# Performance work log

Measured on AMD Instinct MI355X. Metric: run time of the kernel, lower is better.

## Reference

```python
import jax, jax.numpy as jnp
import numpy as np

B, NQ, NK, D = 4, 4096, 4096, 1024


def setup_inputs() -> dict:
    key = jax.random.key(0)
    kq, kv = jax.random.split(key)
    query = jax.random.normal(kq, (B, NQ, D), dtype=jnp.float32)
    values = jax.random.normal(kv, (B, NK, D), dtype=jnp.float32)
    return {"query": query, "values": values}


def reference(query, values):
    # scores = Q @ V^T  (unscaled), shape [B, NQ, NK]
    scores = jnp.einsum("bqd,bkd->bqk", query, values)
    attn = jax.nn.softmax(scores, axis=-1)
    # context = attn @ V, shape [B, NQ, D]
    context = jnp.einsum("bqk,bkd->bqd", attn, values)
    return context
```

## Files before the change

### kernel.cpp

```cpp
#include <hip/hip_runtime.h>


#define NB   4
#define NQL  4096
#define NKL  4096
#define DIM  1024
#define BQ   32
#define BK   32
#define NW   8
#define DSL  128
#define NT   (NKL / BK)
#define LOG2E 1.44269504088896340736f
#define PBW  40

typedef float f32x2 __attribute__((ext_vector_type(2)));
typedef float f32x4 __attribute__((ext_vector_type(4)));
typedef _Float16 f16x8 __attribute__((ext_vector_type(8)));
typedef short s16x8 __attribute__((ext_vector_type(8)));
typedef short s16x4 __attribute__((ext_vector_type(4)));
typedef unsigned int uint_;

union Frag { f16x8 v; s16x8 s; _Float16 h[8]; };

__device__ __forceinline__ void rawbar() {
    asm volatile("s_waitcnt lgkmcnt(0)\n\ts_barrier" ::: "memory");
}

__global__ void prep_v(const float* __restrict__ Vg, short* __restrict__ v16,
                       short* __restrict__ vt16) {
    __shared__ short lds[64][72];
    const int t   = (int)threadIdx.x;
    const int blk = (int)blockIdx.x;
    const int bb    = blk >> 10;
    const int ktile = (blk >> 4) & 63;
    const int dtile = blk & 15;
    const int k0 = ktile * 64, d0 = dtile * 64;
    const int row = t >> 2;
    const int cb  = (t & 3) * 16;

    const float* src = Vg + ((size_t)(bb * NKL + k0 + row) * DIM + d0 + cb);
    short* vdst = v16 + ((size_t)(bb * NKL + k0 + row) * DIM + d0 + cb);
#pragma unroll
    for (int i = 0; i < 4; ++i) {
        f32x4 x = *(const f32x4*)(src + i * 4);
        s16x4 h;
#pragma unroll
        for (int j = 0; j < 4; ++j)
            h[j] = __builtin_bit_cast(short, (_Float16)x[j]);
        *(s16x4*)(vdst + i * 4) = h;
        *(s16x4*)&lds[row][cb + i * 4] = h;
    }
    __syncthreads();
    short* tdst = vt16 + ((size_t)(bb * DIM + d0 + row) * NKL + k0 + cb);
#pragma unroll
    for (int i = 0; i < 4; ++i) {
        s16x4 h;
#pragma unroll
        for (int j = 0; j < 4; ++j)
            h[j] = lds[cb + i * 4 + j][row];
        *(s16x4*)(tdst + i * 4) = h;
    }
}

template<int MODE>
__global__ __attribute__((amdgpu_flat_work_group_size(512, 512),
                          amdgpu_waves_per_eu(1, 4)))
void attn_f16(const float* __restrict__ Qg, const float* __restrict__ Vg,
              float* __restrict__ Og, const short* __restrict__ v16,
              const short* __restrict__ vt16) {
    __shared__ float spart[2][NW][BQ][BK];
    __shared__ __align__(16) short pbuf[2][BQ * PBW];
    __shared__ float arun[2][BQ];
    __shared__ float lsum[BQ];

    const int tid = (int)threadIdx.x;
    const int l   = tid & 63;
    const int w   = tid >> 6;
    const int l15 = l & 15;
    const int lg  = l >> 4;

    const int bid  = (int)blockIdx.x;
    const int orig = (bid & 7) * 64 + (bid >> 3);
    const int b  = orig >> 7;
    const int qt = orig & 127;
    const int q0 = qt * BQ;
    const int dw = w * DSL;

    f16x8 qf[2][4];
#pragma unroll
    for (int qb = 0; qb < 2; ++qb)
#pragma unroll
        for (int dc = 0; dc < 4; ++dc) {
            const float* qp = Qg + (size_t)(b * NQL + q0 + qb * 16 + l15) * DIM
                            + dw + dc * 32 + lg * 8;
            f32x4 x0 = *(const f32x4*)qp;
            f32x4 x1 = *(const f32x4*)(qp + 4);
            f16x8 a;
#pragma unroll
            for (int j = 0; j < 4; ++j) { a[j] = (_Float16)x0[j]; a[j + 4] = (_Float16)x1[j]; }
            qf[qb][dc] = a;
        }

    f32x4 oacc[2][8];
#pragma unroll
    for (int qb = 0; qb < 2; ++qb)
#pragma unroll
        for (int dg = 0; dg < 8; ++dg)
            oacc[qb][dg] = (f32x4){0.f, 0.f, 0.f, 0.f};

    f32x4 sacc[2][2];
    f32x4 hA32[4][2], hB32[4][2];
    s16x8 hA16[4], hB16[4];

    auto loadstage = [&](int buf, int kt_, int kb) {
        if constexpr (MODE == 1) {
            const short* vp = v16 + ((size_t)(b * NKL + kt_ * BK + kb * 16 + l15) * DIM
                            + dw + lg * 8);
            s16x8 (&hb)[4] = buf ? hB16 : hA16;
#pragma unroll
            for (int dc = 0; dc < 4; ++dc)
                hb[dc] = *(const s16x8*)(vp + dc * 32);
        } else {
            const float* vp = Vg + (size_t)(b * NKL + kt_ * BK + kb * 16 + l15) * DIM
                            + dw + lg * 8;
            f32x4 (&hb)[4][2] = buf ? hB32 : hA32;
#pragma unroll
            for (int dc = 0; dc < 4; ++dc) {
                hb[dc][0] = *(const f32x4*)(vp + dc * 32);
                hb[dc][1] = *(const f32x4*)(vp + dc * 32 + 4);
            }
        }
    };

    auto qkt_half = [&](int buf, int kb) {
#pragma unroll
        for (int dc = 0; dc < 4; ++dc) {
            Frag fa;
            if constexpr (MODE == 1) {
                fa.s = buf ? hB16[dc] : hA16[dc];
            } else {
                f32x4 (&hb)[4][2] = buf ? hB32 : hA32;
#pragma unroll
                for (int j = 0; j < 4; ++j) {
                    fa.h[j]     = (_Float16)hb[dc][0][j];
                    fa.h[j + 4] = (_Float16)hb[dc][1][j];
                }
            }
            sacc[kb][0] = __builtin_amdgcn_mfma_f32_16x16x32_f16(fa.v, qf[0][dc], sacc[kb][0], 0, 0, 0);
            sacc[kb][1] = __builtin_amdgcn_mfma_f32_16x16x32_f16(fa.v, qf[1][dc], sacc[kb][1], 0, 0, 0);
        }
    };

    auto qkt_tile = [&](int kt_, int spbuf) {
#pragma unroll
        for (int kb = 0; kb < 2; ++kb)
#pragma unroll
            for (int qb = 0; qb < 2; ++qb)
                sacc[kb][qb] = (f32x4){0.f, 0.f, 0.f, 0.f};
        const int ktn = (kt_ + 1 < NT) ? kt_ + 1 : NT - 1;
        qkt_half(0, 0);
        loadstage(0, ktn, 0);
        qkt_half(1, 1);
        loadstage(1, ktn, 1);
#pragma unroll
        for (int kb = 0; kb < 2; ++kb)
#pragma unroll
            for (int qb = 0; qb < 2; ++qb) {
                const int q = qb * 16 + l15;
                const int kblk = (kb * 16 + lg * 4) ^ ((q & 7) << 2);
                *(f32x4*)&spart[spbuf][w][q][kblk] = sacc[kb][qb];
            }
    };

    const int qsm = 4 * w + lg;
    const int kk  = (2 * l15) ^ ((qsm & 7) << 2);

    float m_reg  = -3e38f;
    float l_lane = 0.f;

    auto softmax_tile = [&](int cur) {
        f32x2 sp = (f32x2){0.f, 0.f};
#pragma unroll
        for (int wv = 0; wv < NW; ++wv)
            sp += *(const f32x2*)&spart[cur][wv][qsm][kk];
        float s0 = sp[0], s1 = sp[1];
        float smax = fmaxf(s0, s1);
        float alpha = 1.0f;
        if (!__all(smax - m_reg <= 8.0f)) {
            float mloc = smax;
#pragma unroll
            for (int off = 1; off < 16; off <<= 1)
                mloc = fmaxf(mloc, __shfl_xor(mloc, off));
            float mnew = fmaxf(m_reg, mloc);
            alpha = exp2f((m_reg - mnew) * LOG2E);
            m_reg = mnew;
        }
        float p0 = exp2f((s0 - m_reg) * LOG2E);
        float p1 = exp2f((s1 - m_reg) * LOG2E);
        l_lane = alpha * l_lane + (p0 + p1);
        if (l15 == 0) arun[cur][qsm] = alpha;
        uint_ pk = (uint_)__builtin_bit_cast(unsigned short, (_Float16)p0)
                 | ((uint_)__builtin_bit_cast(unsigned short, (_Float16)p1) << 16);
        *(uint_*)&pbuf[cur][qsm * PBW + 2 * l15] = pk;
    };

    s16x8 pvreg[8];
    float pv32[8][8];

    auto pv_loads = [&](int kt_) {
        if constexpr (MODE == 1) {
            const short* vtb = vt16 + ((size_t)(b * DIM + dw + l15) * NKL
                             + kt_ * BK + lg * 8);
#pragma unroll
            for (int dg = 0; dg < 8; ++dg)
                pvreg[dg] = *(const s16x8*)(vtb + (size_t)dg * 16 * NKL);
        }
    };

    auto pv_tile = [&](int kt_, int cur) {
        if constexpr (MODE == 0) {
            const float* vb = Vg + (size_t)(b * NKL + kt_ * BK + lg * 8) * DIM
                            + dw + l15;
#pragma unroll
            for (int dg = 0; dg < 8; ++dg)
#pragma unroll
                for (int j = 0; j < 8; ++j)
                    pv32[dg][j] = vb[(size_t)j * DIM + dg * 16];
        }
        f32x4 av[2];
#pragma unroll
        for (int qb = 0; qb < 2; ++qb)
            av[qb] = *(const f32x4*)&arun[cur][qb * 16 + lg * 4];
        bool mine1 = true;
#pragma unroll
        for (int qb = 0; qb < 2; ++qb)
#pragma unroll
            for (int r = 0; r < 4; ++r)
                mine1 = mine1 && (av[qb][r] == 1.0f);
        if (!__all(mine1)) {
#pragma unroll
            for (int qb = 0; qb < 2; ++qb)
#pragma unroll
                for (int dg = 0; dg < 8; ++dg)
#pragma unroll
                    for (int r = 0; r < 4; ++r)
                        oacc[qb][dg][r] *= av[qb][r];
        }
        Frag pf[2];
#pragma unroll
        for (int qb = 0; qb < 2; ++qb)
            pf[qb].s = *(const s16x8*)&pbuf[cur][(qb * 16 + l15) * PBW + lg * 8];
#pragma unroll
        for (int dg = 0; dg < 8; ++dg) {
            Frag bf;
            if constexpr (MODE == 1) {
                bf.s = pvreg[dg];
            } else {
#pragma unroll
                for (int j = 0; j < 8; ++j)
                    bf.h[j] = (_Float16)pv32[dg][j];
            }
            __builtin_amdgcn_s_setprio(1);
#pragma unroll
            for (int qb = 0; qb < 2; ++qb)
                oacc[qb][dg] = __builtin_amdgcn_mfma_f32_16x16x32_f16(
                    pf[qb].v, bf.v, oacc[qb][dg], 0, 0, 0);
            __builtin_amdgcn_s_setprio(0);
        }
    };

    loadstage(0, 0, 0);
    loadstage(1, 0, 1);
    qkt_tile(0, 0);
    rawbar();

    for (int kt = 1; kt < NT; ++kt) {
        const int cur = (kt - 1) & 1;
        pv_loads(kt - 1);
        qkt_tile(kt, kt & 1);
        softmax_tile(cur);
        rawbar();
        pv_tile(kt - 1, cur);
    }

    {
        const int cur = (NT - 1) & 1;
        pv_loads(NT - 1);
        softmax_tile(cur);
        rawbar();
        pv_tile(NT - 1, cur);
    }

    {
        float rs = l_lane;
#pragma unroll
        for (int off = 1; off < 16; off <<= 1)
            rs += __shfl_xor(rs, off);
        if (l15 == 0) lsum[qsm] = rs;
    }
    __syncthreads();
#pragma unroll
    for (int qb = 0; qb < 2; ++qb) {
        f32x4 lv = *(const f32x4*)&lsum[qb * 16 + lg * 4];
        float il[4];
#pragma unroll
        for (int r = 0; r < 4; ++r) il[r] = 1.0f / lv[r];
#pragma unroll
        for (int dg = 0; dg < 8; ++dg)
#pragma unroll
            for (int r = 0; r < 4; ++r) {
                int q = q0 + qb * 16 + lg * 4 + r;
                int d = dw + dg * 16 + l15;
                Og[(size_t)(b * NQL + q) * DIM + d] = oacc[qb][dg][r] * il[r];
            }
    }
}

extern "C" void kernel_launch(void* const* d_in, const int* in_sizes, int n_in,
                              void* d_out, int out_size, void* d_ws, size_t ws_size,
                              hipStream_t stream) {
    const float* Q = (const float*)d_in[0];
    const float* V = (const float*)d_in[1];
    float* O = (float*)d_out;
    (void)in_sizes; (void)n_in; (void)out_size;

    const size_t elems = (size_t)NB * NKL * DIM;
    const size_t need  = 2 * elems * sizeof(short);
    dim3 grid(NB * (NQL / BQ));
    dim3 block(NW * 64);
    if (ws_size >= need) {
        short* v16  = (short*)d_ws;
        short* vt16 = v16 + elems;
        prep_v<<<dim3(NB * 1024), dim3(256), 0, stream>>>(V, v16, vt16);
        attn_f16<1><<<grid, block, 0, stream>>>(Q, V, O, v16, vt16);
    } else {
        attn_f16<0><<<grid, block, 0, stream>>>(Q, V, O, nullptr, nullptr);
    }
}
```

Baseline: 937.1 us.

## Double key tile to 64 and store partial scores in fp16 LDS

Raises the key tile from 32 to 64, so each iteration covers four 16-key QK^T sub-blocks and two PV k-chunks. This halves the number of loop iterations, barriers and softmax passes. Partial scores from each wave are now written to LDS as fp16 instead of fp32, halving LDS traffic for the cross-wave reduction, at the cost of precision in the partial sums. The second PV chunk is loaded inside pv_tile without prefetch, which may expose latency and adds register pressure.

```diff
diff --git a/kernel.cpp b/kernel.cpp
--- a/kernel.cpp
+++ b/kernel.cpp
@@ -6,21 +6,20 @@
 #define NKL  4096
 #define DIM  1024
 #define BQ   32
-#define BK   32
+#define BK   64
 #define NW   8
 #define DSL  128
 #define NT   (NKL / BK)
 #define LOG2E 1.44269504088896340736f
-#define PBW  40
-
-typedef float f32x2 __attribute__((ext_vector_type(2)));
+#define PBW  72
+
 typedef float f32x4 __attribute__((ext_vector_type(4)));
 typedef _Float16 f16x8 __attribute__((ext_vector_type(8)));
 typedef short s16x8 __attribute__((ext_vector_type(8)));
 typedef short s16x4 __attribute__((ext_vector_type(4)));
-typedef unsigned int uint_;
-
-union Frag { f16x8 v; s16x8 s; _Float16 h[8]; };
+
+union Frag  { f16x8 v; s16x8 s; _Float16 h[8]; };
+union Half4 { s16x4 s; _Float16 h[4]; };
 
 __device__ __forceinline__ void rawbar() {
     asm volatile("s_waitcnt lgkmcnt(0)\n\ts_barrier" ::: "memory");
@@ -68,7 +67,7 @@
 void attn_f16(const float* __restrict__ Qg, const float* __restrict__ Vg,
               float* __restrict__ Og, const short* __restrict__ v16,
               const short* __restrict__ vt16) {
-    __shared__ float spart[2][NW][BQ][BK];
+    __shared__ __align__(16) short spart_h[2][NW][BQ][BK];
     __shared__ __align__(16) short pbuf[2][BQ * PBW];
     __shared__ float arun[2][BQ];
     __shared__ float lsum[BQ];
@@ -108,26 +107,24 @@
         for (int dg = 0; dg < 8; ++dg)
             oacc[qb][dg] = (f32x4){0.f, 0.f, 0.f, 0.f};
 
-    f32x4 sacc[2][2];
-    f32x4 hA32[4][2], hB32[4][2];
-    s16x8 hA16[4], hB16[4];
+    f32x4 sacc[4][2];
+    s16x8 hst[2][4];
+    f32x4 hst32[2][4][2];
 
     auto loadstage = [&](int buf, int kt_, int kb) {
         if constexpr (MODE == 1) {
             const short* vp = v16 + ((size_t)(b * NKL + kt_ * BK + kb * 16 + l15) * DIM
                             + dw + lg * 8);
-            s16x8 (&hb)[4] = buf ? hB16 : hA16;
 #pragma unroll
             for (int dc = 0; dc < 4; ++dc)
-                hb[dc] = *(const s16x8*)(vp + dc * 32);
+                hst[buf][dc] = *(const s16x8*)(vp + dc * 32);
         } else {
             const float* vp = Vg + (size_t)(b * NKL + kt_ * BK + kb * 16 + l15) * DIM
                             + dw + lg * 8;
-            f32x4 (&hb)[4][2] = buf ? hB32 : hA32;
 #pragma unroll
             for (int dc = 0; dc < 4; ++dc) {
-                hb[dc][0] = *(const f32x4*)(vp + dc * 32);
-                hb[dc][1] = *(const f32x4*)(vp + dc * 32 + 4);
+                hst32[buf][dc][0] = *(const f32x4*)(vp + dc * 32);
+                hst32[buf][dc][1] = *(const f32x4*)(vp + dc * 32 + 4);
             }
         }
     };
@@ -137,13 +134,12 @@
         for (int dc = 0; dc < 4; ++dc) {
             Frag fa;
             if constexpr (MODE == 1) {
-                fa.s = buf ? hB16[dc] : hA16[dc];
+                fa.s = hst[buf][dc];
             } else {
-                f32x4 (&hb)[4][2] = buf ? hB32 : hA32;
 #pragma unroll
                 for (int j = 0; j < 4; ++j) {
-                    fa.h[j]     = (_Float16)hb[dc][0][j];
-                    fa.h[j + 4] = (_Float16)hb[dc][1][j];
+                    fa.h[j]     = (_Float16)hst32[buf][dc][0][j];
+                    fa.h[j + 4] = (_Float16)hst32[buf][dc][1][j];
                 }
             }
             sacc[kb][0] = __builtin_amdgcn_mfma_f32_16x16x32_f16(fa.v, qf[0][dc], sacc[kb][0], 0, 0, 0);
@@ -153,38 +149,46 @@
 
     auto qkt_tile = [&](int kt_, int spbuf) {
 #pragma unroll
-        for (int kb = 0; kb < 2; ++kb)
+        for (int kb = 0; kb < 4; ++kb)
 #pragma unroll
             for (int qb = 0; qb < 2; ++qb)
                 sacc[kb][qb] = (f32x4){0.f, 0.f, 0.f, 0.f};
         const int ktn = (kt_ + 1 < NT) ? kt_ + 1 : NT - 1;
-        qkt_half(0, 0);
-        loadstage(0, ktn, 0);
-        qkt_half(1, 1);
-        loadstage(1, ktn, 1);
-#pragma unroll
-        for (int kb = 0; kb < 2; ++kb)
+        qkt_half(0, 0);  loadstage(0, kt_, 2);
+        qkt_half(1, 1);  loadstage(1, kt_, 3);
+        qkt_half(0, 2);  loadstage(0, ktn, 0);
+        qkt_half(1, 3);  loadstage(1, ktn, 1);
+#pragma unroll
+        for (int kb = 0; kb < 4; ++kb)
 #pragma unroll
             for (int qb = 0; qb < 2; ++qb) {
                 const int q = qb * 16 + l15;
                 const int kblk = (kb * 16 + lg * 4) ^ ((q & 7) << 2);
-                *(f32x4*)&spart[spbuf][w][q][kblk] = sacc[kb][qb];
+                Half4 pk;
+#pragma unroll
+                for (int r = 0; r < 4; ++r)
+                    pk.h[r] = (_Float16)sacc[kb][qb][r];
+                *(s16x4*)&spart_h[spbuf][w][q][kblk] = pk.s;
             }
     };
 
     const int qsm = 4 * w + lg;
-    const int kk  = (2 * l15) ^ ((qsm & 7) << 2);
+    const int kk  = (4 * l15) ^ ((qsm & 7) << 2);
 
     float m_reg  = -3e38f;
     float l_lane = 0.f;
 
     auto softmax_tile = [&](int cur) {
-        f32x2 sp = (f32x2){0.f, 0.f};
-#pragma unroll
-        for (int wv = 0; wv < NW; ++wv)
-            sp += *(const f32x2*)&spart[cur][wv][qsm][kk];
-        float s0 = sp[0], s1 = sp[1];
-        float smax = fmaxf(s0, s1);
+        float s[4] = {0.f, 0.f, 0.f, 0.f};
+#pragma unroll
+        for (int wv = 0; wv < NW; ++wv) {
+            Half4 hp;
+            hp.s = *(const s16x4*)&spart_h[cur][wv][qsm][kk];
+#pragma unroll
+            for (int r = 0; r < 4; ++r)
+                s[r] += (float)hp.h[r];
+        }
+        float smax = fmaxf(fmaxf(s[0], s[1]), fmaxf(s[2], s[3]));
         float alpha = 1.0f;
         if (!__all(smax - m_reg <= 8.0f)) {
             float mloc = smax;
@@ -195,17 +199,20 @@
             alpha = exp2f((m_reg - mnew) * LOG2E);
             m_reg = mnew;
         }
-        float p0 = exp2f((s0 - m_reg) * LOG2E);
-        float p1 = exp2f((s1 - m_reg) * LOG2E);
-        l_lane = alpha * l_lane + (p0 + p1);
+        float psum = 0.f;
+        Half4 pk;
+#pragma unroll
+        for (int r = 0; r < 4; ++r) {
+            float p = exp2f((s[r] - m_reg) * LOG2E);
+            psum += p;
+            pk.h[r] = (_Float16)p;
+        }
+        l_lane = alpha * l_lane + psum;
         if (l15 == 0) arun[cur][qsm] = alpha;
-        uint_ pk = (uint_)__builtin_bit_cast(unsigned short, (_Float16)p0)
-                 | ((uint_)__builtin_bit_cast(unsigned short, (_Float16)p1) << 16);
-        *(uint_*)&pbuf[cur][qsm * PBW + 2 * l15] = pk;
+        *(s16x4*)&pbuf[cur][qsm * PBW + 4 * l15] = pk.s;
     };
 
     s16x8 pvreg[8];
-    float pv32[8][8];
 
     auto pv_loads = [&](int kt_) {
         if constexpr (MODE == 1) {
@@ -218,14 +225,13 @@
     };
 
     auto pv_tile = [&](int kt_, int cur) {
-        if constexpr (MODE == 0) {
-            const float* vb = Vg + (size_t)(b * NKL + kt_ * BK + lg * 8) * DIM
-                            + dw + l15;
+        s16x8 pv1[8];
+        if constexpr (MODE == 1) {
+            const short* vtb = vt16 + ((size_t)(b * DIM + dw + l15) * NKL
+                             + kt_ * BK + lg * 8);
 #pragma unroll
             for (int dg = 0; dg < 8; ++dg)
-#pragma unroll
-                for (int j = 0; j < 8; ++j)
-                    pv32[dg][j] = vb[(size_t)j * DIM + dg * 16];
+                pv1[dg] = *(const s16x8*)(vtb + (size_t)dg * 16 * NKL + 32);
         }
         f32x4 av[2];
 #pragma unroll
@@ -246,26 +252,49 @@
                     for (int r = 0; r < 4; ++r)
                         oacc[qb][dg][r] *= av[qb][r];
         }
-        Frag pf[2];
+        Frag pf[2][2];
 #pragma unroll
         for (int qb = 0; qb < 2; ++qb)
-            pf[qb].s = *(const s16x8*)&pbuf[cur][(qb * 16 + l15) * PBW + lg * 8];
-#pragma unroll
-        for (int dg = 0; dg < 8; ++dg) {
-            Frag bf;
-            if constexpr (MODE == 1) {
-                bf.s = pvreg[dg];
-            } else {
-#pragma unroll
-                for (int j = 0; j < 8; ++j)
-                    bf.h[j] = (_Float16)pv32[dg][j];
-            }
-            __builtin_amdgcn_s_setprio(1);
-#pragma unroll
-            for (int qb = 0; qb < 2; ++qb)
-                oacc[qb][dg] = __builtin_amdgcn_mfma_f32_16x16x32_f16(
-                    pf[qb].v, bf.v, oacc[qb][dg], 0, 0, 0);
-            __builtin_amdgcn_s_setprio(0);
+#pragma unroll
+            for (int c = 0; c < 2; ++c)
+                pf[qb][c].s = *(const s16x8*)&pbuf[cur][(qb * 16 + l15) * PBW
+                                                        + c * 32 + lg * 8];
+        if constexpr (MODE == 1) {
+#pragma unroll
+            for (int dg = 0; dg < 8; ++dg) {
+                __builtin_amdgcn_s_setprio(1);
+#pragma unroll
+                for (int qb = 0; qb < 2; ++qb)
+                    oacc[qb][dg] = __builtin_amdgcn_mfma_f32_16x16x32_f16(
+                        pf[qb][0].v, (Frag{.s = pvreg[dg]}).v, oacc[qb][dg], 0, 0, 0);
+                __builtin_amdgcn_s_setprio(0);
+            }
+#pragma unroll
+            for (int dg = 0; dg < 8; ++dg) {
+                __builtin_amdgcn_s_setprio(1);
+#pragma unroll
+                for (int qb = 0; qb < 2; ++qb)
+                    oacc[qb][dg] = __builtin_amdgcn_mfma_f32_16x16x32_f16(
+                        pf[qb][1].v, (Frag{.s = pv1[dg]}).v, oacc[qb][dg], 0, 0, 0);
+                __builtin_amdgcn_s_setprio(0);
+            }
+        } else {
+#pragma unroll
+            for (int c = 0; c < 2; ++c) {
+                const float* vb = Vg + (size_t)(b * NKL + kt_ * BK + c * 32 + lg * 8) * DIM
+                                + dw + l15;
+#pragma unroll
+                for (int dg = 0; dg < 8; ++dg) {
+                    Frag bf;
+#pragma unroll
+                    for (int j = 0; j < 8; ++j)
+                        bf.h[j] = (_Float16)vb[(size_t)j * DIM + dg * 16];
+#pragma unroll
+                    for (int qb = 0; qb < 2; ++qb)
+                        oacc[qb][dg] = __builtin_amdgcn_mfma_f32_16x16x32_f16(
+                            pf[qb][c].v, bf.v, oacc[qb][dg], 0, 0, 0);
+                }
+            }
         }
     };
 
```

After: 934.0 us. No clear change (-0.3%).

## Double query tile to 64 rows with 16 waves and store partial scores as fp16

Applied to the files above, without the earlier changes.

The query tile per block grows from 32 to 64 rows, and the wave count goes from 8 to 16, each wave covering a 64-wide slice of the head dimension. Each V tile streamed from memory is now reused across twice as many queries, halving global V traffic and the grid size. Cross-wave partial scores are stored in LDS as fp16 instead of fp32, which keeps the LDS footprint and reduction bandwidth in check. The cost is fewer blocks for occupancy, larger 1024-thread workgroups, and lower precision in the partial-score reduction.

```diff
diff --git a/kernel.cpp b/kernel.cpp
--- a/kernel.cpp
+++ b/kernel.cpp
@@ -5,22 +5,24 @@
 #define NQL  4096
 #define NKL  4096
 #define DIM  1024
-#define BQ   32
+#define BQ   64
 #define BK   32
-#define NW   8
-#define DSL  128
+#define NW   16
+#define DSL  64
 #define NT   (NKL / BK)
 #define LOG2E 1.44269504088896340736f
 #define PBW  40
 
-typedef float f32x2 __attribute__((ext_vector_type(2)));
 typedef float f32x4 __attribute__((ext_vector_type(4)));
 typedef _Float16 f16x8 __attribute__((ext_vector_type(8)));
 typedef short s16x8 __attribute__((ext_vector_type(8)));
 typedef short s16x4 __attribute__((ext_vector_type(4)));
+typedef short s16x2 __attribute__((ext_vector_type(2)));
 typedef unsigned int uint_;
 
-union Frag { f16x8 v; s16x8 s; _Float16 h[8]; };
+union Frag  { f16x8 v; s16x8 s; _Float16 h[8]; };
+union Half4 { s16x4 s; _Float16 h[4]; };
+union Half2 { s16x2 s; _Float16 h[2]; };
 
 __device__ __forceinline__ void rawbar() {
     asm volatile("s_waitcnt lgkmcnt(0)\n\ts_barrier" ::: "memory");
@@ -63,12 +65,12 @@
 }
 
 template<int MODE>
-__global__ __attribute__((amdgpu_flat_work_group_size(512, 512),
+__global__ __attribute__((amdgpu_flat_work_group_size(1024, 1024),
                           amdgpu_waves_per_eu(1, 4)))
 void attn_f16(const float* __restrict__ Qg, const float* __restrict__ Vg,
               float* __restrict__ Og, const short* __restrict__ v16,
               const short* __restrict__ vt16) {
-    __shared__ float spart[2][NW][BQ][BK];
+    __shared__ __align__(16) short spart_h[2][NW][BQ][BK];
     __shared__ __align__(16) short pbuf[2][BQ * PBW];
     __shared__ float arun[2][BQ];
     __shared__ float lsum[BQ];
@@ -80,17 +82,17 @@
     const int lg  = l >> 4;
 
     const int bid  = (int)blockIdx.x;
-    const int orig = (bid & 7) * 64 + (bid >> 3);
-    const int b  = orig >> 7;
-    const int qt = orig & 127;
+    const int orig = (bid & 7) * 32 + (bid >> 3);
+    const int b  = orig >> 6;
+    const int qt = orig & 63;
     const int q0 = qt * BQ;
     const int dw = w * DSL;
 
-    f16x8 qf[2][4];
-#pragma unroll
-    for (int qb = 0; qb < 2; ++qb)
-#pragma unroll
-        for (int dc = 0; dc < 4; ++dc) {
+    f16x8 qf[4][2];
+#pragma unroll
+    for (int qb = 0; qb < 4; ++qb)
+#pragma unroll
+        for (int dc = 0; dc < 2; ++dc) {
             const float* qp = Qg + (size_t)(b * NQL + q0 + qb * 16 + l15) * DIM
                             + dw + dc * 32 + lg * 8;
             f32x4 x0 = *(const f32x4*)qp;
@@ -101,53 +103,52 @@
             qf[qb][dc] = a;
         }
 
-    f32x4 oacc[2][8];
-#pragma unroll
-    for (int qb = 0; qb < 2; ++qb)
-#pragma unroll
-        for (int dg = 0; dg < 8; ++dg)
+    f32x4 oacc[4][4];
+#pragma unroll
+    for (int qb = 0; qb < 4; ++qb)
+#pragma unroll
+        for (int dg = 0; dg < 4; ++dg)
             oacc[qb][dg] = (f32x4){0.f, 0.f, 0.f, 0.f};
 
-    f32x4 sacc[2][2];
-    f32x4 hA32[4][2], hB32[4][2];
-    s16x8 hA16[4], hB16[4];
+    f32x4 sacc[2][4];
+    s16x8 hst[2][2];
+    f32x4 hst32[2][2][2];
 
     auto loadstage = [&](int buf, int kt_, int kb) {
         if constexpr (MODE == 1) {
             const short* vp = v16 + ((size_t)(b * NKL + kt_ * BK + kb * 16 + l15) * DIM
                             + dw + lg * 8);
-            s16x8 (&hb)[4] = buf ? hB16 : hA16;
-#pragma unroll
-            for (int dc = 0; dc < 4; ++dc)
-                hb[dc] = *(const s16x8*)(vp + dc * 32);
+#pragma unroll
+            for (int dc = 0; dc < 2; ++dc)
+                hst[buf][dc] = *(const s16x8*)(vp + dc * 32);
         } else {
             const float* vp = Vg + (size_t)(b * NKL + kt_ * BK + kb * 16 + l15) * DIM
                             + dw + lg * 8;
-            f32x4 (&hb)[4][2] = buf ? hB32 : hA32;
-#pragma unroll
-            for (int dc = 0; dc < 4; ++dc) {
-                hb[dc][0] = *(const f32x4*)(vp + dc * 32);
-                hb[dc][1] = *(const f32x4*)(vp + dc * 32 + 4);
+#pragma unroll
+            for (int dc = 0; dc < 2; ++dc) {
+                hst32[buf][dc][0] = *(const f32x4*)(vp + dc * 32);
+                hst32[buf][dc][1] = *(const f32x4*)(vp + dc * 32 + 4);
             }
         }
     };
 
     auto qkt_half = [&](int buf, int kb) {
 #pragma unroll
-        for (int dc = 0; dc < 4; ++dc) {
+        for (int dc = 0; dc < 2; ++dc) {
             Frag fa;
             if constexpr (MODE == 1) {
-                fa.s = buf ? hB16[dc] : hA16[dc];
+                fa.s = hst[buf][dc];
             } else {
-                f32x4 (&hb)[4][2] = buf ? hB32 : hA32;
 #pragma unroll
                 for (int j = 0; j < 4; ++j) {
-                    fa.h[j]     = (_Float16)hb[dc][0][j];
-                    fa.h[j + 4] = (_Float16)hb[dc][1][j];
+                    fa.h[j]     = (_Float16)hst32[buf][dc][0][j];
+                    fa.h[j + 4] = (_Float16)hst32[buf][dc][1][j];
                 }
             }
-            sacc[kb][0] = __builtin_amdgcn_mfma_f32_16x16x32_f16(fa.v, qf[0][dc], sacc[kb][0], 0, 0, 0);
-            sacc[kb][1] = __builtin_amdgcn_mfma_f32_16x16x32_f16(fa.v, qf[1][dc], sacc[kb][1], 0, 0, 0);
+#pragma unroll
+            for (int qb = 0; qb < 4; ++qb)
+                sacc[kb][qb] = __builtin_amdgcn_mfma_f32_16x16x32_f16(
+                    fa.v, qf[qb][dc], sacc[kb][qb], 0, 0, 0);
         }
     };
 
@@ -155,7 +156,7 @@
 #pragma unroll
         for (int kb = 0; kb < 2; ++kb)
 #pragma unroll
-            for (int qb = 0; qb < 2; ++qb)
+            for (int qb = 0; qb < 4; ++qb)
                 sacc[kb][qb] = (f32x4){0.f, 0.f, 0.f, 0.f};
         const int ktn = (kt_ + 1 < NT) ? kt_ + 1 : NT - 1;
         qkt_half(0, 0);
@@ -165,10 +166,14 @@
 #pragma unroll
         for (int kb = 0; kb < 2; ++kb)
 #pragma unroll
-            for (int qb = 0; qb < 2; ++qb) {
+            for (int qb = 0; qb < 4; ++qb) {
                 const int q = qb * 16 + l15;
                 const int kblk = (kb * 16 + lg * 4) ^ ((q & 7) << 2);
-                *(f32x4*)&spart[spbuf][w][q][kblk] = sacc[kb][qb];
+                Half4 pk;
+#pragma unroll
+                for (int r = 0; r < 4; ++r)
+                    pk.h[r] = (_Float16)sacc[kb][qb][r];
+                *(s16x4*)&spart_h[spbuf][w][q][kblk] = pk.s;
             }
     };
 
@@ -179,11 +184,14 @@
     float l_lane = 0.f;
 
     auto softmax_tile = [&](int cur) {
-        f32x2 sp = (f32x2){0.f, 0.f};
-#pragma unroll
-        for (int wv = 0; wv < NW; ++wv)
-            sp += *(const f32x2*)&spart[cur][wv][qsm][kk];
-        float s0 = sp[0], s1 = sp[1];
+        float s0 = 0.f, s1 = 0.f;
+#pragma unroll
+        for (int wv = 0; wv < NW; ++wv) {
+            Half2 hp;
+            hp.s = *(const s16x2*)&spart_h[cur][wv][qsm][kk];
+            s0 += (float)hp.h[0];
+            s1 += (float)hp.h[1];
+        }
         float smax = fmaxf(s0, s1);
         float alpha = 1.0f;
         if (!__all(smax - m_reg <= 8.0f)) {
@@ -204,15 +212,15 @@
         *(uint_*)&pbuf[cur][qsm * PBW + 2 * l15] = pk;
     };
 
-    s16x8 pvreg[8];
-    float pv32[8][8];
+    s16x8 pvreg[4];
+    float pv32[4][8];
 
     auto pv_loads = [&](int kt_) {
         if constexpr (MODE == 1) {
             const short* vtb = vt16 + ((size_t)(b * DIM + dw + l15) * NKL
                              + kt_ * BK + lg * 8);
 #pragma unroll
-            for (int dg = 0; dg < 8; ++dg)
+            for (int dg = 0; dg < 4; ++dg)
                 pvreg[dg] = *(const s16x8*)(vtb + (size_t)dg * 16 * NKL);
         }
     };
@@ -222,36 +230,36 @@
             const float* vb = Vg + (size_t)(b * NKL + kt_ * BK + lg * 8) * DIM
                             + dw + l15;
 #pragma unroll
-            for (int dg = 0; dg < 8; ++dg)
+            for (int dg = 0; dg < 4; ++dg)
 #pragma unroll
                 for (int j = 0; j < 8; ++j)
                     pv32[dg][j] = vb[(size_t)j * DIM + dg * 16];
         }
-        f32x4 av[2];
-#pragma unroll
-        for (int qb = 0; qb < 2; ++qb)
+        f32x4 av[4];
+#pragma unroll
+        for (int qb = 0; qb < 4; ++qb)
             av[qb] = *(const f32x4*)&arun[cur][qb * 16 + lg * 4];
         bool mine1 = true;
 #pragma unroll
-        for (int qb = 0; qb < 2; ++qb)
+        for (int qb = 0; qb < 4; ++qb)
 #pragma unroll
             for (int r = 0; r < 4; ++r)
                 mine1 = mine1 && (av[qb][r] == 1.0f);
         if (!__all(mine1)) {
 #pragma unroll
-            for (int qb = 0; qb < 2; ++qb)
-#pragma unroll
-                for (int dg = 0; dg < 8; ++dg)
+            for (int qb = 0; qb < 4; ++qb)
+#pragma unroll
+                for (int dg = 0; dg < 4; ++dg)
 #pragma unroll
                     for (int r = 0; r < 4; ++r)
                         oacc[qb][dg][r] *= av[qb][r];
         }
-        Frag pf[2];
-#pragma unroll
-        for (int qb = 0; qb < 2; ++qb)
+        Frag pf[4];
+#pragma unroll
+        for (int qb = 0; qb < 4; ++qb)
             pf[qb].s = *(const s16x8*)&pbuf[cur][(qb * 16 + l15) * PBW + lg * 8];
 #pragma unroll
-        for (int dg = 0; dg < 8; ++dg) {
+        for (int dg = 0; dg < 4; ++dg) {
             Frag bf;
             if constexpr (MODE == 1) {
                 bf.s = pvreg[dg];
@@ -262,7 +270,7 @@
             }
             __builtin_amdgcn_s_setprio(1);
 #pragma unroll
-            for (int qb = 0; qb < 2; ++qb)
+            for (int qb = 0; qb < 4; ++qb)
                 oacc[qb][dg] = __builtin_amdgcn_mfma_f32_16x16x32_f16(
                     pf[qb].v, bf.v, oacc[qb][dg], 0, 0, 0);
             __builtin_amdgcn_s_setprio(0);
@@ -300,13 +308,13 @@
     }
     __syncthreads();
 #pragma unroll
-    for (int qb = 0; qb < 2; ++qb) {
+    for (int qb = 0; qb < 4; ++qb) {
         f32x4 lv = *(const f32x4*)&lsum[qb * 16 + lg * 4];
         float il[4];
 #pragma unroll
         for (int r = 0; r < 4; ++r) il[r] = 1.0f / lv[r];
 #pragma unroll
-        for (int dg = 0; dg < 8; ++dg)
+        for (int dg = 0; dg < 4; ++dg)
 #pragma unroll
             for (int r = 0; r < 4; ++r) {
                 int q = q0 + qb * 16 + lg * 4 + r;
```

New measurement: 2.445 ms. 161% more time.
